# Performance work log

Measured on AMD Instinct MI355X. Metric: run time of the kernel, lower is better.

The kernel has to match this reference:

```python
import jax, jax.numpy as jnp
import numpy as np

B, S, HID = 2, 2048, 2048
H, HK, D = 16, 4, 128  # num_heads, num_kv_heads, head_dim
G = H // HK            # GQA group size


def _make_rope(B, S, D):
    pos = jnp.arange(S, dtype=jnp.float32)
    inv_freq = 1.0 / (10000.0 ** (jnp.arange(0, D, 2, dtype=jnp.float32) / D))
    freqs = pos[:, None] * inv_freq[None, :]          # [S, D/2]
    emb = jnp.concatenate([freqs, freqs], axis=-1)     # [S, D]
    cos = jnp.broadcast_to(jnp.cos(emb)[None], (B, S, D))
    sin = jnp.broadcast_to(jnp.sin(emb)[None], (B, S, D))
    return cos, sin


def setup_inputs() -> dict:
    key = jax.random.key(0)
    k0, k1, k2 = jax.random.split(key, 3)
    hidden_states = jax.random.normal(k0, (B, S, HID), dtype=jnp.float32)
    cos, sin = _make_rope(B, S, D)
    w_qkv = jax.random.normal(k1, ((H + 2 * HK) * D, HID), dtype=jnp.float32) * 0.02
    b_qkv = jnp.zeros(((H + 2 * HK) * D,), dtype=jnp.float32)
    w_o = jax.random.normal(k2, (HID, HID), dtype=jnp.float32) * 0.02
    b_o = jnp.zeros((HID,), dtype=jnp.float32)
    return {"hidden_states": hidden_states, "cos": cos, "sin": sin,
            "w_qkv": w_qkv, "b_qkv": b_qkv, "w_o": w_o, "b_o": b_o}


def _rotate_half(x):
    x1, x2 = jnp.split(x, 2, axis=-1)
    return jnp.concatenate([-x2, x1], axis=-1)


def reference(hidden_states, cos, sin, w_qkv, b_qkv, w_o, b_o):
    b, s, _ = hidden_states.shape
    qkv = jnp.einsum('bsh,oh->bso', hidden_states, w_qkv) + b_qkv
    q, k, v = jnp.split(qkv, [H * D, (H + HK) * D], axis=-1)
    # [B, heads, S, D]
    q = q.reshape(b, s, H, D).transpose(0, 2, 1, 3)
    k = k.reshape(b, s, HK, D).transpose(0, 2, 1, 3)
    v = v.reshape(b, s, HK, D).transpose(0, 2, 1, 3)
    # RoPE (cos/sin broadcast over head axis)
    c = cos[:, None, :, :]
    sn = sin[:, None, :, :]
    q = q * c + _rotate_half(q) * sn
    k = k * c + _rotate_half(k) * sn
    # GQA attention without materializing repeated K/V: group q heads
    qg = q.reshape(b, HK, G, s, D)
    scale = 1.0 / jnp.sqrt(jnp.float32(D))
    scores = jnp.einsum('bkgqd,bkpd->bkgqp', qg, k) * scale  # [B,HK,G,S,S]
    probs = jax.nn.softmax(scores, axis=-1)
    out = jnp.einsum('bkgqp,bkpd->bkgqd', probs, v)           # [B,HK,G,S,D]
    out = out.reshape(b, H, s, D).transpose(0, 2, 1, 3).reshape(b, s, H * D)
    return jnp.einsum('bsh,oh->bso', out, w_o) + b_o
```

## Files before the change

kernel.cpp:

```cpp
#include <hip/hip_runtime.h>
#include <hip/hip_bf16.h>
#include <stdint.h>

typedef __bf16 bf16x8 __attribute__((ext_vector_type(8)));
typedef float f32x4 __attribute__((ext_vector_type(4)));
typedef float f32x16 __attribute__((ext_vector_type(16)));
typedef float f32x4v __attribute__((ext_vector_type(4)));
typedef unsigned short u16;
typedef unsigned int u32;
typedef u16 u16x8 __attribute__((ext_vector_type(8)));
typedef u32 u32x4 __attribute__((ext_vector_type(4)));

#define B_ 2
#define S_ 2048
#define HID_ 2048
#define H_ 16
#define HK_ 4
#define D_ 128
#define NQKV_ 3072

__device__ __forceinline__ u16 f2bf(float f) {
  u32 u = __builtin_bit_cast(u32, f);
  u32 r = (u + 0x7fffu + ((u >> 16) & 1u)) >> 16;
  return (u16)r;
}
__device__ __forceinline__ float bf2f(u16 v) {
  u32 u = ((u32)v) << 16;
  return __builtin_bit_cast(float, u);
}
__device__ __forceinline__ u32 cvtpk(float lo, float hi) {
  u32 r;
  asm("v_cvt_pk_bf16_f32 %0, %1, %2" : "=v"(r) : "v"(lo), "v"(hi));
  return r;
}
__device__ __forceinline__ void gload_lds16(const void* g, void* l) {
  __builtin_amdgcn_global_load_lds((const __attribute__((address_space(1))) void*)g,
                                   (__attribute__((address_space(3))) void*)l, 16, 0, 0);
}

__global__ __launch_bounds__(256) void k_cvt3(const float* __restrict__ a, u16* __restrict__ oa, int na,
                                              const float* __restrict__ b, u16* __restrict__ ob, int nb,
                                              const float* __restrict__ c, u16* __restrict__ oc, int nc) {
  int total = na + nb + nc;
  for (int i = blockIdx.x * 256 + threadIdx.x; i < total; i += gridDim.x * 256) {
    const float* src;
    u16* dst;
    int j = i;
    if (j < na) { src = a; dst = oa; }
    else if (j < na + nb) { j -= na; src = b; dst = ob; }
    else { j -= na + nb; src = c; dst = oc; }
    const f32x4v* p = (const f32x4v*)(src + (size_t)j * 8);
    f32x4v x = p[0], y = p[1];
    u16x8 w;
    w[0] = f2bf(x[0]); w[1] = f2bf(x[1]); w[2] = f2bf(x[2]); w[3] = f2bf(x[3]);
    w[4] = f2bf(y[0]); w[5] = f2bf(y[1]); w[6] = f2bf(y[2]); w[7] = f2bf(y[3]);
    *(u16x8*)(dst + (size_t)j * 8) = w;
  }
}

template <int ISSUES>
__device__ __forceinline__ void stage_half(const u16* __restrict__ src, int K, char* ldsb, int tid) {
#pragma unroll
  for (int i = 0; i < ISSUES; ++i) {
    int off = i * 8192 + tid * 16;
    int r = off >> 7, cb = off & 127;
    int scb = cb ^ ((r & 7) << 4);
    gload_lds16((const char*)(src + (size_t)r * K) + scb, ldsb + i * 8192 + (tid & ~63) * 16);
  }
}

template <int BM, typename CT>
__global__ __launch_bounds__(512, 1) void k_gemm8p(const u16* __restrict__ A, const u16* __restrict__ Bm,
                                                   const float* __restrict__ bias, CT* __restrict__ C,
                                                   int M, int N, int K) {
  constexpr int HAR = BM / 2;
  constexpr int AHB = HAR * 128;
  constexpr int AISS = AHB / 8192;
  constexpr int MREP = BM / 32;
  constexpr int MQ = MREP / 4;
  constexpr int DB = 2 * AHB + 32768;
  __shared__ __attribute__((aligned(16))) char lds[2 * DB];
  const int tid = threadIdx.x, lane = tid & 63;
  const int wid = tid >> 6, wm = wid >> 2, wn = wid & 3;
  const int l15 = lane & 15, l4 = lane >> 4;
  const int nwg = gridDim.x * gridDim.y;
  const int bid = blockIdx.y * gridDim.x + blockIdx.x;
  const int wgid = (bid & 7) * (nwg >> 3) + (bid >> 3);
  const int bx = wgid % gridDim.x, by = wgid / gridDim.x;
  const int row0 = by * BM, col0 = bx * 256;
  const int NT = K >> 6;

  f32x4 acc[MREP][4] = {};

  auto stageA = [&](int t, int h) {
    stage_half<AISS>(A + (size_t)(row0 + h * HAR) * K + t * 64, K, lds + (t & 1) * DB + h * AHB, tid);
  };
  auto stageB = [&](int t, int h) {
    stage_half<2>(Bm + (size_t)(col0 + h * 128) * K + t * 64, K, lds + (t & 1) * DB + 2 * AHB + h * 16384, tid);
  };

  stageA(0, 0); stageA(0, 1); stageB(0, 0); stageB(0, 1);
  if (NT > 1) { stageB(1, 0); stageB(1, 1); }
  if (NT > 1) asm volatile("s_waitcnt vmcnt(4)" ::: "memory");
  else        asm volatile("s_waitcnt vmcnt(0)" ::: "memory");
  __builtin_amdgcn_s_barrier();

  const char* myA = lds + wm * AHB;
  const char* myB = lds + 2 * AHB + (wn >> 1) * 16384;
  const int rBb = (wn & 1) * 64;

  for (int t = 0; t < NT; ++t) {
    const int d = t & 1;
    const char* Ab = myA + d * DB;
    const char* Bb = myB + d * DB;
    bf16x8 bfr[4][2];
#pragma unroll
    for (int j = 0; j < 4; ++j) {
      if (j == 0) {
#pragma unroll
        for (int n = 0; n < 4; ++n)
#pragma unroll
          for (int ks = 0; ks < 2; ++ks) {
            int r = rBb + n * 16 + l15;
            bfr[n][ks] = *(const bf16x8*)(Bb + r * 128 + ((ks * 64 + l4 * 16) ^ ((r & 7) << 4)));
          }
      }
      bf16x8 afr[MQ][2];
#pragma unroll
      for (int mq = 0; mq < MQ; ++mq)
#pragma unroll
        for (int ks = 0; ks < 2; ++ks) {
          int r = (j * MQ + mq) * 16 + l15;
          afr[mq][ks] = *(const bf16x8*)(Ab + r * 128 + ((ks * 64 + l4 * 16) ^ ((r & 7) << 4)));
        }
      if (j == 0) { if (t + 1 < NT) stageA(t + 1, 0); }
      else if (j == 1) { if (t + 1 < NT) stageA(t + 1, 1); }
      else if (j == 2) { if (t + 2 < NT) stageB(t + 2, 0); }
      else {
        if (t + 2 < NT) { stageB(t + 2, 1); asm volatile("s_waitcnt vmcnt(4)" ::: "memory"); }
        else             asm volatile("s_waitcnt vmcnt(0)" ::: "memory");
      }
      __builtin_amdgcn_s_barrier();
      asm volatile("s_waitcnt lgkmcnt(0)" ::: "memory");
      __builtin_amdgcn_s_setprio(1);
#pragma unroll
      for (int mq = 0; mq < MQ; ++mq)
#pragma unroll
        for (int ks = 0; ks < 2; ++ks)
#pragma unroll
          for (int n = 0; n < 4; ++n)
            acc[j * MQ + mq][n] =
                __builtin_amdgcn_mfma_f32_16x16x32_bf16(afr[mq][ks], bfr[n][ks], acc[j * MQ + mq][n], 0, 0, 0);
      __builtin_amdgcn_s_setprio(0);
      __builtin_amdgcn_s_barrier();
    }
  }

#pragma unroll
  for (int m = 0; m < MREP; ++m) {
    int grow = row0 + wm * HAR + m * 16 + l4 * 4;
#pragma unroll
    for (int n = 0; n < 4; ++n) {
      int gcol = col0 + wn * 64 + n * 16 + l15;
      float bv = bias[gcol];
#pragma unroll
      for (int r2 = 0; r2 < 4; ++r2) {
        float v = acc[m][n][r2] + bv;
        if constexpr (sizeof(CT) == 2) C[(size_t)(grow + r2) * N + gcol] = (CT)f2bf(v);
        else                           C[(size_t)(grow + r2) * N + gcol] = v;
      }
    }
  }
}

__global__ __launch_bounds__(256) void k_rope_split(const u16* __restrict__ qkv,
                                                    const float* __restrict__ cosb,
                                                    const float* __restrict__ sinb,
                                                    u16* __restrict__ Qb, u16* __restrict__ Kb,
                                                    u16* __restrict__ Vt) {
  const int bs = blockIdx.x;
  const int b = bs >> 11, s = bs & 2047;
  const size_t base = (size_t)bs * NQKV_;
  const size_t cs = (size_t)bs * D_;
  const int tid = threadIdx.x;
  const float qscale = 0.08838834764831845f;

  if (tid < 160) {
    const bool isq = tid < 128;
    const int idx = isq ? tid : (tid - 128);
    const int hh = idx >> 3, d0 = (idx & 7) * 8;
    const size_t srcb = base + (isq ? 0 : H_ * D_) + hh * D_;
    bf16x8 x1 = *(const bf16x8*)(qkv + srcb + d0);
    bf16x8 x2 = *(const bf16x8*)(qkv + srcb + d0 + 64);
    u16x8 y1, y2;
    const u16x8 u1 = __builtin_bit_cast(u16x8, x1);
    const u16x8 u2 = __builtin_bit_cast(u16x8, x2);
    const float sc = isq ? qscale : 1.0f;
#pragma unroll
    for (int i = 0; i < 8; ++i) {
      float f1 = bf2f(u1[i]), f2 = bf2f(u2[i]);
      float c1 = cosb[cs + d0 + i], s1 = sinb[cs + d0 + i];
      float c2 = cosb[cs + 64 + d0 + i], s2 = sinb[cs + 64 + d0 + i];
      y1[i] = f2bf((f1 * c1 - f2 * s1) * sc);
      y2[i] = f2bf((f2 * c2 + f1 * s2) * sc);
    }
    size_t o;
    if (isq) o = ((size_t)(b * H_ + hh) * S_ + s) * D_ + d0;
    else     o = ((size_t)(b * HK_ + hh) * S_ + s) * D_ + d0;
    u16* dst = isq ? Qb : Kb;
    *(u16x8*)(dst + o) = y1;
    *(u16x8*)(dst + o + 64) = y2;
  } else if (tid < 224) {
    const int idx = tid - 160;
    const int hk = idx >> 4, d0 = (idx & 15) * 8;
    bf16x8 xv = *(const bf16x8*)(qkv + base + (H_ + HK_) * D_ + hk * D_ + d0);
    const u16x8 uv = __builtin_bit_cast(u16x8, xv);
    u16* vb = Vt + (size_t)(b * HK_ + hk) * D_ * S_ + s;
#pragma unroll
    for (int i = 0; i < 8; ++i) vb[(size_t)(d0 + i) * S_] = uv[i];
  }
}

__global__ __launch_bounds__(512, 2) void k_attn(const u16* __restrict__ Qb, const u16* __restrict__ Kb,
                                                 const u16* __restrict__ Vt, u16* __restrict__ Ob) {
  __shared__ __attribute__((aligned(16))) char lds[66560];
  const int qt = blockIdx.x;
  const int bh = blockIdx.y;
  const int b = bh >> 4, h = bh & 15, hk = h >> 2;
  const int tid = threadIdx.x, lane = tid & 63, wid = tid >> 6;
  const int l31 = lane & 31, hi = lane >> 5;
  const int g = wid >> 2, wq = wid & 3;

  const int qrow = qt * 128 + wq * 32 + l31;
  const u16* qptr = Qb + ((size_t)(b * H_ + h) * S_ + qrow) * D_;
  bf16x8 qf[8];
#pragma unroll
  for (int ks = 0; ks < 8; ++ks) qf[ks] = *(const bf16x8*)(qptr + ks * 16 + hi * 8);

  const char* kB = (const char*)(Kb + (size_t)(b * HK_ + hk) * S_ * D_);
  const char* vB = (const char*)(Vt + (size_t)(b * HK_ + hk) * D_ * S_);
  char* gbase = lds + g * 32768;

  int koff[4], voff[4];
#pragma unroll
  for (int i = 0; i < 4; ++i) {
    int c = wq * 256 + i * 64 + lane;
    int row = c >> 4, u = c & 15;
    koff[i] = row * 256 + ((u ^ (row & 15)) << 4);
    int d = c >> 3, uv = c & 7;
    voff[i] = d * (S_ * 2) + ((uv ^ (d & 7)) << 4);
  }

  auto stage = [&](int tt) {
#pragma unroll
    for (int i = 0; i < 4; ++i)
      gload_lds16(kB + (size_t)tt * 16384 + koff[i], gbase + wq * 4096 + i * 1024);
#pragma unroll
    for (int i = 0; i < 4; ++i)
      gload_lds16(vB + (size_t)tt * 128 + voff[i], gbase + 16384 + wq * 4096 + i * 1024);
  };

  f32x16 o[4] = {};
  float mrun = -1e30f, lrun = 0.f;

  const int tt0 = g * 16;
  stage(tt0);
  __syncthreads();

  for (int t = 0; t < 16; ++t) {
    f32x16 sc[2] = {};
    __builtin_amdgcn_s_setprio(1);
#pragma unroll
    for (int ks = 0; ks < 8; ++ks) {
#pragma unroll
      for (int T = 0; T < 2; ++T) {
        int row = T * 32 + l31;
        bf16x8 kf = *(const bf16x8*)(gbase + ((row * 256 + ks * 32 + hi * 16) ^ ((row & 15) << 4)));
        sc[T] = __builtin_amdgcn_mfma_f32_32x32x16_bf16(kf, qf[ks], sc[T], 0, 0, 0);
      }
    }
    __builtin_amdgcn_s_setprio(0);

    float pmax = sc[0][0];
#pragma unroll
    for (int r = 1; r < 16; ++r) pmax = fmaxf(pmax, sc[0][r]);
#pragma unroll
    for (int r = 0; r < 16; ++r) pmax = fmaxf(pmax, sc[1][r]);
    pmax = fmaxf(pmax, __shfl_xor(pmax, 32));
    if (__any(pmax > mrun + 8.f)) {
      float mn = fmaxf(mrun, pmax);
      float alpha = __expf(mrun - mn);
      mrun = mn;
      lrun *= alpha;
#pragma unroll
      for (int dt = 0; dt < 4; ++dt)
#pragma unroll
        for (int r = 0; r < 16; ++r) o[dt][r] *= alpha;
    }
    float rs = 0.f;
#pragma unroll
    for (int T = 0; T < 2; ++T)
#pragma unroll
      for (int r = 0; r < 16; ++r) {
        float p = __expf(sc[T][r] - mrun);
        sc[T][r] = p;
        rs += p;
      }
    rs += __shfl_xor(rs, 32);
    lrun += rs;

    bf16x8 pf[4];
#pragma unroll
    for (int T = 0; T < 2; ++T) {
#pragma unroll
      for (int gg = 0; gg < 2; ++gg) {
        u32 a0 = cvtpk(sc[T][8 * gg + 0], sc[T][8 * gg + 1]);
        u32 a1 = cvtpk(sc[T][8 * gg + 2], sc[T][8 * gg + 3]);
        u32 a2 = cvtpk(sc[T][8 * gg + 4], sc[T][8 * gg + 5]);
        u32 a3 = cvtpk(sc[T][8 * gg + 6], sc[T][8 * gg + 7]);
        u32 x0 = (u32)__shfl_xor((int)a0, 32);
        u32 x1 = (u32)__shfl_xor((int)a1, 32);
        u32 x2 = (u32)__shfl_xor((int)a2, 32);
        u32 x3 = (u32)__shfl_xor((int)a3, 32);
        u32 s0 = hi ? x2 : a0;
        u32 s1 = hi ? x3 : a1;
        u32 s2 = hi ? a2 : x0;
        u32 s3 = hi ? a3 : x1;
        u32x4 w = {s0, s1, s2, s3};
        pf[T * 2 + gg] = __builtin_bit_cast(bf16x8, w);
      }
    }

    __builtin_amdgcn_s_setprio(1);
#pragma unroll
    for (int ks2 = 0; ks2 < 4; ++ks2) {
#pragma unroll
      for (int dt = 0; dt < 4; ++dt) {
        int row = dt * 32 + l31;
        bf16x8 vf = *(const bf16x8*)(gbase + 16384 + ((row * 128 + ks2 * 32 + hi * 16) ^ ((row & 7) << 4)));
        o[dt] = __builtin_amdgcn_mfma_f32_32x32x16_bf16(vf, pf[ks2], o[dt], 0, 0, 0);
      }
    }
    __builtin_amdgcn_s_setprio(0);

    __syncthreads();
    if (t < 15) stage(tt0 + t + 1);
    __syncthreads();
  }

  float2* mlb = (float2*)(lds + 65536);
  if (g == 1) {
    char* ob = lds + wq * 16384;
#pragma unroll
    for (int dt = 0; dt < 4; ++dt)
#pragma unroll
      for (int r = 0; r < 4; ++r) {
        f32x4 w = {o[dt][4 * r + 0], o[dt][4 * r + 1], o[dt][4 * r + 2], o[dt][4 * r + 3]};
        *(f32x4*)(ob + ((size_t)((dt * 4 + r) * 64 + lane)) * 16) = w;
      }
    if (!hi) mlb[wq * 32 + l31] = float2{mrun, lrun};
  }
  __syncthreads();
  float inv = 0.f;
  if (g == 0) {
    float2 ml1 = mlb[wq * 32 + l31];
    float m = fmaxf(mrun, ml1.x);
    float a0 = __expf(mrun - m), a1 = __expf(ml1.x - m);
    float lt = lrun * a0 + ml1.y * a1;
    char* ob = lds + wq * 16384;
#pragma unroll
    for (int dt = 0; dt < 4; ++dt)
#pragma unroll
      for (int r = 0; r < 4; ++r) {
        f32x4 c1 = *(const f32x4*)(ob + ((size_t)((dt * 4 + r) * 64 + lane)) * 16);
#pragma unroll
        for (int j = 0; j < 4; ++j) o[dt][4 * r + j] = o[dt][4 * r + j] * a0 + c1[j] * a1;
      }
    inv = 1.0f / lt;
  }
  __syncthreads();

  if (g == 0) {
    char* myreg = lds + wq * 8192;
#pragma unroll
    for (int dt = 0; dt < 4; ++dt)
#pragma unroll
      for (int t = 0; t < 8; ++t) {
        u32 w = cvtpk(o[dt][2 * t] * inv, o[dt][2 * t + 1] * inv);
        int d0 = dt * 32 + 2 * (t & 1) + 8 * (t >> 1) + 4 * hi;
        *(u32*)(myreg + ((l31 * 256 + d0 * 2) ^ ((l31 & 15) << 4))) = w;
      }
    asm volatile("s_waitcnt lgkmcnt(0)");
    {
      int q = lane >> 1, hf = lane & 1;
      int srow = qt * 128 + wq * 32 + q;
      u16* orow = Ob + ((size_t)(b * S_ + srow)) * HID_ + h * 128 + hf * 64;
#pragma unroll
      for (int i = 0; i < 8; ++i) {
        bf16x8 vv = *(const bf16x8*)(myreg + ((q * 256 + hf * 128 + i * 16) ^ ((q & 15) << 4)));
        *(bf16x8*)(orow + i * 8) = vv;
      }
    }
  }
}

extern "C" void kernel_launch(void* const* d_in, const int* in_sizes, int n_in,
                              void* d_out, int out_size, void* d_ws, size_t ws_size,
                              hipStream_t stream) {
  const float* hs = (const float*)d_in[0];
  const float* cosb = (const float*)d_in[1];
  const float* sinb = (const float*)d_in[2];
  const float* w_qkv = (const float*)d_in[3];
  const float* b_qkv = (const float*)d_in[4];
  const float* w_o = (const float*)d_in[5];
  const float* b_o = (const float*)d_in[6];
  float* out = (float*)d_out;

  char* ws = (char*)d_ws;
  u16* Xb    = (u16*)ws;
  u16* Wqkvb = (u16*)(ws + 16777216);
  u16* Wob   = (u16*)(ws + 29360128);
  u16* qkvb  = (u16*)(ws + 37748736);
  u16* Qb    = (u16*)(ws + 62914560);
  u16* Kb    = (u16*)(ws + 79691776);
  u16* Vt    = (u16*)(ws + 83886080);
  u16* Ob = Xb;

  hipLaunchKernelGGL(k_cvt3, dim3(2048), dim3(256), 0, stream,
                     hs, Xb, (B_ * S_ * HID_) / 8,
                     w_qkv, Wqkvb, (NQKV_ * HID_) / 8,
                     w_o, Wob, (HID_ * HID_) / 8);
  hipLaunchKernelGGL((k_gemm8p<256, u16>), dim3(NQKV_ / 256, (B_ * S_) / 256), dim3(512), 0, stream,
                     Xb, Wqkvb, b_qkv, qkvb, B_ * S_, NQKV_, HID_);
  hipLaunchKernelGGL(k_rope_split, dim3(B_ * S_), dim3(256), 0, stream, qkvb, cosb, sinb, Qb, Kb, Vt);
  hipLaunchKernelGGL(k_attn, dim3(S_ / 128, B_ * H_), dim3(512), 0, stream, Qb, Kb, Vt, Ob);
  hipLaunchKernelGGL((k_gemm8p<128, float>), dim3(HID_ / 256, (B_ * S_) / 128), dim3(512), 0, stream,
                     Ob, Wob, b_o, out, B_ * S_, HID_, HID_);
}
```

Before: 232.0 us.

## Prefetch K/V tiles into registers and shrink LDS with bf16 merge buffer

Replaces direct global-to-LDS async loads with register prefetch: the next K/V tile is loaded into registers at the top of each iteration and written to swizzled LDS after the compute barrier, overlapping global latency with the MFMA work. The cross-group partial-output merge now stores bf16 instead of fp32, which lets the LDS allocation drop to 64KB, possibly improving occupancy. It costs extra VGPRs for the prefetch registers and some precision in the partial output merge.

```diff
diff --git a/kernel.cpp b/kernel.cpp
--- a/kernel.cpp
+++ b/kernel.cpp
@@ -223,7 +223,7 @@
 
 __global__ __launch_bounds__(512, 2) void k_attn(const u16* __restrict__ Qb, const u16* __restrict__ Kb,
                                                  const u16* __restrict__ Vt, u16* __restrict__ Ob) {
-  __shared__ __attribute__((aligned(16))) char lds[66560];
+  __shared__ __attribute__((aligned(16))) char lds[65536];
   const int qt = blockIdx.x;
   const int bh = blockIdx.y;
   const int b = bh >> 4, h = bh & 15, hk = h >> 2;
@@ -237,37 +237,45 @@
 #pragma unroll
   for (int ks = 0; ks < 8; ++ks) qf[ks] = *(const bf16x8*)(qptr + ks * 16 + hi * 8);
 
-  const char* kB = (const char*)(Kb + (size_t)(b * HK_ + hk) * S_ * D_);
-  const char* vB = (const char*)(Vt + (size_t)(b * HK_ + hk) * D_ * S_);
+  const u16* kbase = Kb + (size_t)(b * HK_ + hk) * S_ * D_;
+  const u16* vbase = Vt + (size_t)(b * HK_ + hk) * D_ * S_;
   char* gbase = lds + g * 32768;
 
-  int koff[4], voff[4];
+  int krow[4], kc[4], vrow[4], vc[4];
 #pragma unroll
   for (int i = 0; i < 4; ++i) {
-    int c = wq * 256 + i * 64 + lane;
-    int row = c >> 4, u = c & 15;
-    koff[i] = row * 256 + ((u ^ (row & 15)) << 4);
-    int d = c >> 3, uv = c & 7;
-    voff[i] = d * (S_ * 2) + ((uv ^ (d & 7)) << 4);
-  }
-
-  auto stage = [&](int tt) {
-#pragma unroll
-    for (int i = 0; i < 4; ++i)
-      gload_lds16(kB + (size_t)tt * 16384 + koff[i], gbase + wq * 4096 + i * 1024);
-#pragma unroll
-    for (int i = 0; i < 4; ++i)
-      gload_lds16(vB + (size_t)tt * 128 + voff[i], gbase + 16384 + wq * 4096 + i * 1024);
-  };
+    int s = (tid & 255) + i * 256;
+    krow[i] = s >> 4; kc[i] = s & 15;
+    vrow[i] = s >> 3; vc[i] = s & 7;
+  }
 
   f32x16 o[4] = {};
   float mrun = -1e30f, lrun = 0.f;
 
-  const int tt0 = g * 16;
-  stage(tt0);
+  bf16x8 kreg[4], vreg[4];
+  auto load_tile = [&](int tt) {
+#pragma unroll
+    for (int i = 0; i < 4; ++i) {
+      kreg[i] = *(const bf16x8*)(kbase + (size_t)(tt * 64 + krow[i]) * D_ + kc[i] * 8);
+      vreg[i] = *(const bf16x8*)(vbase + (size_t)vrow[i] * S_ + tt * 64 + vc[i] * 8);
+    }
+  };
+  auto write_tile = [&]() {
+#pragma unroll
+    for (int i = 0; i < 4; ++i) {
+      *(bf16x8*)(gbase + ((krow[i] * 256 + kc[i] * 16) ^ ((krow[i] & 15) << 4))) = kreg[i];
+      *(bf16x8*)(gbase + 16384 + ((vrow[i] * 128 + vc[i] * 16) ^ ((vrow[i] & 7) << 4))) = vreg[i];
+    }
+  };
+
+  const int t0 = g * 16;
+  load_tile(t0);
+  write_tile();
   __syncthreads();
 
   for (int t = 0; t < 16; ++t) {
+    if (t < 15) load_tile(t0 + t + 1);
+
     f32x16 sc[2] = {};
     __builtin_amdgcn_s_setprio(1);
 #pragma unroll
@@ -344,20 +352,18 @@
     __builtin_amdgcn_s_setprio(0);
 
     __syncthreads();
-    if (t < 15) stage(tt0 + t + 1);
+    if (t < 15) write_tile();
     __syncthreads();
   }
 
-  float2* mlb = (float2*)(lds + 65536);
+  float2* mlb = (float2*)(lds + 32768);
   if (g == 1) {
-    char* ob = lds + wq * 16384;
+    char* myp = lds + wq * 8192;
 #pragma unroll
     for (int dt = 0; dt < 4; ++dt)
 #pragma unroll
-      for (int r = 0; r < 4; ++r) {
-        f32x4 w = {o[dt][4 * r + 0], o[dt][4 * r + 1], o[dt][4 * r + 2], o[dt][4 * r + 3]};
-        *(f32x4*)(ob + ((size_t)((dt * 4 + r) * 64 + lane)) * 16) = w;
-      }
+      for (int t = 0; t < 8; ++t)
+        *(u32*)(myp + (dt * 8 + t) * 256 + lane * 4) = cvtpk(o[dt][2 * t], o[dt][2 * t + 1]);
     if (!hi) mlb[wq * 32 + l31] = float2{mrun, lrun};
   }
   __syncthreads();
@@ -367,16 +373,18 @@
     float m = fmaxf(mrun, ml1.x);
     float a0 = __expf(mrun - m), a1 = __expf(ml1.x - m);
     float lt = lrun * a0 + ml1.y * a1;
-    char* ob = lds + wq * 16384;
+    inv = 1.0f / lt;
+    char* myp = lds + wq * 8192;
 #pragma unroll
     for (int dt = 0; dt < 4; ++dt)
 #pragma unroll
-      for (int r = 0; r < 4; ++r) {
-        f32x4 c1 = *(const f32x4*)(ob + ((size_t)((dt * 4 + r) * 64 + lane)) * 16);
-#pragma unroll
-        for (int j = 0; j < 4; ++j) o[dt][4 * r + j] = o[dt][4 * r + j] * a0 + c1[j] * a1;
-      }
-    inv = 1.0f / lt;
+      for (int t = 0; t < 8; ++t) {
+        u32 w = *(const u32*)(myp + (dt * 8 + t) * 256 + lane * 4);
+        float plo = bf2f((u16)(w & 0xffffu));
+        float phi = bf2f((u16)(w >> 16));
+        o[dt][2 * t]     = o[dt][2 * t] * a0 + plo * a1;
+        o[dt][2 * t + 1] = o[dt][2 * t + 1] * a0 + phi * a1;
+      }
   }
   __syncthreads();
 
```

New measurement: 228.4 us. No clear change (-1.5%).
